# Performance work log

Hardware: AMD Instinct MI355X
Metric: run time of the kernel (lower is better)

The kernel has to match this reference:

```python
import jax, jax.numpy as jnp
import numpy as np

DIM = 256
DT_REF = 1.0
EPS = 1e-7
GATE_MIN, GATE_MAX = 0.01, 0.99


def _safe_forcing(exp_arg):
    # expm1(z)/z with denominator regularized by sign of real part (matches torch _safe_forcing)
    safe_denom = exp_arg + EPS * jnp.sign(exp_arg.real + EPS)
    return (jnp.exp(exp_arg) - 1.0) / safe_denom


def setup_inputs() -> dict:
    key = jax.random.key(0)
    ks = jax.random.split(key, 12)
    B, T, D = 8, 4096, DIM
    x_mean_seq = jax.random.normal(ks[0], (B, T, D), dtype=jnp.float32)
    dt_seq = jax.random.uniform(ks[1], (B, T), dtype=jnp.float32)
    # GlobalFluxTracker params
    decay_re = jax.random.normal(ks[2], (D,), dtype=jnp.float32) * 0.1 - 1.0
    decay_im = jax.random.normal(ks[3], (D,), dtype=jnp.float32) * 0.1
    W_in = jax.random.normal(ks[4], (2 * D, 2 * D), dtype=jnp.float32) * (1.0 / np.sqrt(2 * D))
    b_in = jnp.zeros((2 * D,), dtype=jnp.float32)
    W_out = jax.random.normal(ks[5], (2 * D, 2 * D), dtype=jnp.float32) * (1.0 / np.sqrt(2 * D))
    b_out = jnp.zeros((2 * D,), dtype=jnp.float32)
    W_gate = jax.random.normal(ks[6], (D, 2 * D), dtype=jnp.float32) * (1.0 / np.sqrt(2 * D))
    b_gate = jnp.zeros((D,), dtype=jnp.float32)
    # TemporalPropagator diagonal generator params
    lam_re = jax.random.normal(ks[7], (D,), dtype=jnp.float32) * 0.01
    lam_im = jax.random.normal(ks[8], (D,), dtype=jnp.float32) * 0.1
    return {
        "x_mean_seq": x_mean_seq, "dt_seq": dt_seq,
        "decay_re": decay_re, "decay_im": decay_im,
        "W_in": W_in, "b_in": b_in, "W_out": W_out, "b_out": b_out,
        "W_gate": W_gate, "b_gate": b_gate,
        "lam_re": lam_re, "lam_im": lam_im,
    }


def reference(x_mean_seq, dt_seq, decay_re, decay_im, W_in, b_in,
              W_out, b_out, W_gate, b_gate, lam_re, lam_im):
    # dt ratio [B,T,1]
    dt_ratio = (dt_seq / DT_REF)[..., None]

    # --- GlobalFluxTracker.get_scan_operators ---
    lam_f = -jax.nn.softplus(decay_re) + 1j * decay_im          # [D] complex64
    exp_arg = lam_f[None, None, :] * dt_ratio                    # [B,T,D]
    decay = jnp.exp(exp_arg)                                     # [B,T,D]
    forcing = _safe_forcing(exp_arg)                             # [B,T,D]

    # _mix_input on real input (imag part is zero)
    x_cat = jnp.concatenate([x_mean_seq, jnp.zeros_like(x_mean_seq)], axis=-1)
    x_in = x_cat @ W_in.T + b_in                                 # [B,T,2D]
    x_re, x_im = jnp.split(x_in, 2, axis=-1)
    x_mixed = x_re + 1j * x_im                                   # [B,T,D]
    X_scan = x_mixed * forcing                                   # [B,T,D]

    # --- linear recurrence flux_t = decay_t * flux_{t-1} + X_t (associative scan over T) ---
    def combine(c1, c2):
        a1, b1 = c1
        a2, b2 = c2
        return (a1 * a2, b1 * a2 + b2)
    _, flux = jax.lax.associative_scan(combine, (decay, X_scan), axis=1)  # [B,T,D]

    # --- compute_output_seq ---
    s_cat = jnp.concatenate([flux.real, flux.imag], axis=-1)     # [B,T,2D]
    src = s_cat @ W_out.T + b_out
    src_re, src_im = jnp.split(src, 2, axis=-1)
    gate = jax.nn.sigmoid(s_cat @ W_gate.T + b_gate)
    gate = gate * (GATE_MAX - GATE_MIN) + GATE_MIN               # [B,T,D]

    # --- TemporalPropagator.get_transition_operators_seq ---
    lam_p = -jax.nn.softplus(lam_re) + 1j * lam_im
    exp_arg_p = lam_p[None, None, :] * dt_ratio
    decay_p = jnp.exp(exp_arg_p)
    forcing_p = _safe_forcing(exp_arg_p)

    out = jnp.concatenate([
        src_re, src_im, gate,
        decay_p.real, decay_p.imag, forcing_p.real, forcing_p.imag,
    ], axis=-1)                                                  # [B,T,7D]
    return out
```

## Files before the change

kernel.cpp:

```cpp
#include <hip/hip_runtime.h>
#include <math.h>

#define DD 256
#define TT 4096
#define NBATCH 8
#define BTOK 32768
#define EPSF 1e-7f

typedef __attribute__((ext_vector_type(4))) float f32x4;
typedef __attribute__((ext_vector_type(8))) short bf16x8;

__device__ __forceinline__ float softplusf(float x) {
  float e = __expf(-fabsf(x));
  return fmaxf(x, 0.f) + __logf(1.f + e);
}
__device__ __forceinline__ float bf2f(unsigned short u) {
  union { unsigned int i; float f; } v; v.i = ((unsigned int)u) << 16; return v.f;
}
__device__ __forceinline__ unsigned short f2bf(float f) {
  union { float f; unsigned int i; } v; v.f = f;
  unsigned int x = v.i;
  unsigned int lsb = (x >> 16) & 1u;
  x += 0x7fffu + lsb;
  return (unsigned short)(x >> 16);
}
__device__ __forceinline__ void decay_forcing(float are, float aim,
    float& dre, float& dim, float& fre, float& fim) {
  float e = __expf(are);
  float s = __sinf(aim), c = __cosf(aim);
  dre = e * c; dim = e * s;
  float sg = (are + EPSF >= 0.f) ? 1.f : -1.f;
  float denr = are + EPSF * sg;
  float deni = aim;
  float inv = __builtin_amdgcn_rcpf(denr * denr + deni * deni);
  float nr = dre - 1.f, ni = dim;
  fre = (nr * denr + ni * deni) * inv;
  fim = (ni * denr - nr * deni) * inv;
}
__device__ __forceinline__ void gl_lds16(const void* g, void* l) {
  __builtin_amdgcn_global_load_lds(
      (const __attribute__((address_space(1))) unsigned int*)g,
      (__attribute__((address_space(3))) unsigned int*)l, 16, 0, 0);
}

__global__ __launch_bounds__(256) void prep(
    const float* __restrict__ x, unsigned short* __restrict__ Xb,
    const float* __restrict__ Win, unsigned short* __restrict__ Wp1,
    const float* __restrict__ Wout, const float* __restrict__ Wgate,
    unsigned short* __restrict__ Wp3)
{
  const int bid = blockIdx.x;
  if (bid < 8192) {
    size_t i = ((size_t)bid * 256 + threadIdx.x) * 4;
    float4 v = *reinterpret_cast<const float4*>(&x[i]);
    ushort4 u;
    u.x = f2bf(v.x); u.y = f2bf(v.y); u.z = f2bf(v.z); u.w = f2bf(v.w);
    *reinterpret_cast<ushort4*>(&Xb[i]) = u;
  } else if (bid < 8704) {
    const int p = bid - 8192;
    const int k = threadIdx.x;
    const int g = p >> 5, r = p & 31;
    const int src = (r < 16) ? (g * 16 + r) : (256 + g * 16 + (r - 16));
    Wp1[(size_t)p * 256 + k] = f2bf(Win[(size_t)src * 512 + k]);
  } else {
    const int p = bid - 8704;
    const float* src = (p < 512) ? (Wout + (size_t)p * 512)
                                 : (Wgate + (size_t)(p - 512) * 512);
    Wp3[(size_t)p * 512 + threadIdx.x] = f2bf(src[threadIdx.x]);
    Wp3[(size_t)p * 512 + threadIdx.x + 256] = f2bf(src[threadIdx.x + 256]);
  }
}

__global__ __launch_bounds__(256) void k1_mfma(
    const unsigned short* __restrict__ Xb,
    const unsigned short* __restrict__ Wp,
    const float* __restrict__ bin, const float* __restrict__ dts,
    const float* __restrict__ decr, const float* __restrict__ deci,
    unsigned int* __restrict__ Xri)
{
  __shared__ __align__(16) unsigned short As[128 * 64];
  __shared__ __align__(16) unsigned short Bs[128 * 64];
  const int bx = blockIdx.x;
  const int wg = (bx & 7) * 128 + (bx >> 3);
  const int mt = wg >> 2, nt = wg & 3;
  const int m0 = mt * 128, n0 = nt * 128;
  const int tid = threadIdx.x;
  const int lane = tid & 63, wid = tid >> 6;
  const int wr = wid >> 1, wc = wid & 1;
  const int l15 = lane & 15, hi = lane >> 4;
  const int lrow = tid >> 3;
  const int sslot = (tid & 7) ^ (lrow & 7);
  f32x4 acc[4][4];
  f32x4 z = {0.f, 0.f, 0.f, 0.f};
#pragma unroll
  for (int i = 0; i < 4; ++i)
#pragma unroll
    for (int j = 0; j < 4; ++j) acc[i][j] = z;

  for (int k0 = 0; k0 < 256; k0 += 64) {
    __syncthreads();
#pragma unroll
    for (int c = 0; c < 4; ++c) {
      gl_lds16(&Xb[(size_t)(m0 + c * 32 + lrow) * 256 + k0 + sslot * 8],
               &As[c * 2048 + tid * 8]);
      gl_lds16(&Wp[(size_t)(n0 + c * 32 + lrow) * 256 + k0 + sslot * 8],
               &Bs[c * 2048 + tid * 8]);
    }
    __syncthreads();
#pragma unroll
    for (int kk = 0; kk < 2; ++kk) {
      bf16x8 af[4], bfr[4];
      const int rslot = ((kk * 4 + hi) ^ (l15 & 7)) * 8;
#pragma unroll
      for (int m = 0; m < 4; ++m)
        af[m] = *reinterpret_cast<const bf16x8*>(&As[(wr * 64 + m * 16 + l15) * 64 + rslot]);
#pragma unroll
      for (int n = 0; n < 4; ++n)
        bfr[n] = *reinterpret_cast<const bf16x8*>(&Bs[(wc * 64 + n * 16 + l15) * 64 + rslot]);
#pragma unroll
      for (int m = 0; m < 4; ++m)
#pragma unroll
        for (int n = 0; n < 4; ++n)
          acc[m][n] = __builtin_amdgcn_mfma_f32_16x16x32_bf16(af[m], bfr[n], acc[m][n], 0, 0, 0);
    }
  }

  const int pbase = n0 + wc * 64;
#pragma unroll
  for (int pr = 0; pr < 2; ++pr) {
    const int d = (pbase >> 1) + pr * 16 + l15;
    const float nre = -softplusf(decr[d]);
    const float di = deci[d];
    const float br = bin[d], bi = bin[d + 256];
#pragma unroll
    for (int m = 0; m < 4; ++m) {
#pragma unroll
      for (int r = 0; r < 4; ++r) {
        const int row = m0 + wr * 64 + m * 16 + hi * 4 + r;
        float xr = acc[m][2 * pr][r] + br;
        float xi = acc[m][2 * pr + 1][r] + bi;
        float dt = dts[row];
        float are = nre * dt, aim = di * dt;
        float dr_, dm_, fr_, fm_;
        decay_forcing(are, aim, dr_, dm_, fr_, fm_);
        unsigned int pk = (unsigned int)f2bf(xr * fr_ - xi * fm_)
                        | ((unsigned int)f2bf(xr * fm_ + xi * fr_) << 16);
        Xri[(size_t)row * DD + d] = pk;
      }
    }
  }
}

__global__ __launch_bounds__(256) void k2a_chunk(
    const unsigned int* __restrict__ Xri,
    const float* __restrict__ dts, const float* __restrict__ decr,
    const float* __restrict__ deci,
    float4* __restrict__ ops)
{
  const int bx = blockIdx.x;
  const int b = bx >> 6, c = bx & 63;
  const int d = threadIdx.x;
  __shared__ float sdt[64];
  if (threadIdx.x < 64) sdt[threadIdx.x] = dts[b * TT + c * 64 + threadIdx.x];
  const float nre = -softplusf(decr[d]);
  const float di = deci[d];
  __syncthreads();
  float Ar = 1.f, Ai = 0.f, Br = 0.f, Bi = 0.f;
  size_t base = (size_t)(b * TT + c * 64) * DD + d;
  for (int i = 0; i < 64; ++i) {
    float dt = sdt[i];
    float e = __expf(nre * dt);
    float s = __sinf(di * dt), cs = __cosf(di * dt);
    float ar = e * cs, ai = e * s;
    unsigned int pk = Xri[base]; base += DD;
    float xr = bf2f((unsigned short)(pk & 0xffffu));
    float xi = bf2f((unsigned short)(pk >> 16));
    float nAr = Ar * ar - Ai * ai, nAi = Ar * ai + Ai * ar;
    Ar = nAr; Ai = nAi;
    float nBr = Br * ar - Bi * ai + xr, nBi = Br * ai + Bi * ar + xi;
    Br = nBr; Bi = nBi;
  }
  ops[(size_t)bx * DD + d] = make_float4(Ar, Ai, Br, Bi);
}

__global__ __launch_bounds__(256) void k2c_apply(
    const unsigned int* __restrict__ Xri,
    const float* __restrict__ dts, const float* __restrict__ decr,
    const float* __restrict__ deci,
    const float4* __restrict__ ops,
    unsigned short* __restrict__ F)
{
  const int bx = blockIdx.x;
  const int b = bx >> 6, c = bx & 63;
  const int d = threadIdx.x;
  __shared__ float sdt[64];
  if (threadIdx.x < 64) sdt[threadIdx.x] = dts[b * TT + c * 64 + threadIdx.x];
  const float nre = -softplusf(decr[d]);
  const float di = deci[d];
  __syncthreads();

  float hr = 0.f, hi2 = 0.f;
  const size_t obase = (size_t)(b * 64) * DD + d;
  for (int c0 = 0; c0 < c; c0 += 8) {
    float4 oo[8];
#pragma unroll
    for (int j = 0; j < 8; ++j)
      oo[j] = (c0 + j < c) ? ops[obase + (size_t)(c0 + j) * DD]
                           : make_float4(1.f, 0.f, 0.f, 0.f);
#pragma unroll
    for (int j = 0; j < 8; ++j) {
      float nr = oo[j].x * hr - oo[j].y * hi2 + oo[j].z;
      float ni = oo[j].x * hi2 + oo[j].y * hr + oo[j].w;
      hr = nr; hi2 = ni;
    }
  }

  const int tok0 = b * TT + c * 64;
  size_t base = (size_t)tok0 * DD + d;
  for (int i = 0; i < 64; ++i) {
    float dt = sdt[i];
    float e = __expf(nre * dt);
    float s = __sinf(di * dt), cs = __cosf(di * dt);
    float ar = e * cs, ai = e * s;
    unsigned int pk = Xri[base]; base += DD;
    float xr = bf2f((unsigned short)(pk & 0xffffu));
    float xi = bf2f((unsigned short)(pk >> 16));
    float nr = ar * hr - ai * hi2 + xr;
    float ni = ar * hi2 + ai * hr + xi;
    hr = nr; hi2 = ni;
    size_t fb = (size_t)(tok0 + i) * 512 + d;
    F[fb] = f2bf(hr);
    F[fb + 256] = f2bf(hi2);
  }
}

__global__ __launch_bounds__(256) void k3k4(
    const unsigned short* __restrict__ F,
    const unsigned short* __restrict__ Wp,
    const float* __restrict__ bout, const float* __restrict__ bgate,
    const float* __restrict__ dts, const float* __restrict__ lre,
    const float* __restrict__ lim,
    float* __restrict__ out)
{
  __shared__ __align__(16) unsigned short As[128 * 64];
  __shared__ __align__(16) unsigned short Bs[128 * 64];

  const int q = blockIdx.x / 5, r5 = blockIdx.x % 5;

  if (r5 >= 3) {
    const int pb = q * 2 + (r5 - 3);
    const int d = threadIdx.x;
    const float nl = -softplusf(lre[d]);
    const float li = lim[d];
    const int tok0 = pb * 32;
#pragma unroll 4
    for (int i = 0; i < 32; ++i) {
      const int tok = tok0 + i;
      float dt = dts[tok];
      float dr, dm, fr, fm;
      decay_forcing(nl * dt, li * dt, dr, dm, fr, fm);
      float* o = out + (size_t)tok * 1792 + 768;
      o[d] = dr; o[256 + d] = dm; o[512 + d] = fr; o[768 + d] = fm;
    }
    return;
  }

  const int gw = q * 3 + r5;
  const int wg = (gw & 7) * 192 + (gw >> 3);
  const int mt = wg / 6, nt = wg % 6;
  const int m0 = mt * 128, n0 = nt * 128;
  const int tid = threadIdx.x;
  const int lane = tid & 63, wid = tid >> 6;
  const int wr = wid >> 1, wc = wid & 1;
  const int l15 = lane & 15, hi = lane >> 4;
  const int lrow = tid >> 3;
  const int sslot = (tid & 7) ^ (lrow & 7);
  f32x4 acc[4][4];
  f32x4 z = {0.f, 0.f, 0.f, 0.f};
#pragma unroll
  for (int i = 0; i < 4; ++i)
#pragma unroll
    for (int j = 0; j < 4; ++j) acc[i][j] = z;

  for (int k0 = 0; k0 < 512; k0 += 64) {
    __syncthreads();
#pragma unroll
    for (int c = 0; c < 4; ++c) {
      gl_lds16(&F[(size_t)(m0 + c * 32 + lrow) * 512 + k0 + sslot * 8],
               &As[c * 2048 + tid * 8]);
      gl_lds16(&Wp[(size_t)(n0 + c * 32 + lrow) * 512 + k0 + sslot * 8],
               &Bs[c * 2048 + tid * 8]);
    }
    __syncthreads();
#pragma unroll
    for (int kk = 0; kk < 2; ++kk) {
      bf16x8 af[4], bfr[4];
      const int rslot = ((kk * 4 + hi) ^ (l15 & 7)) * 8;
#pragma unroll
      for (int m = 0; m < 4; ++m)
        af[m] = *reinterpret_cast<const bf16x8*>(&As[(wr * 64 + m * 16 + l15) * 64 + rslot]);
#pragma unroll
      for (int n = 0; n < 4; ++n)
        bfr[n] = *reinterpret_cast<const bf16x8*>(&Bs[(wc * 64 + n * 16 + l15) * 64 + rslot]);
#pragma unroll
      for (int m = 0; m < 4; ++m)
#pragma unroll
        for (int n = 0; n < 4; ++n)
          acc[m][n] = __builtin_amdgcn_mfma_f32_16x16x32_bf16(af[m], bfr[n], acc[m][n], 0, 0, 0);
    }
  }

  const int nb = n0 + wc * 64;
  if (nb < 512) {
#pragma unroll
    for (int j = 0; j < 4; ++j) {
      const int col = nb + j * 16 + l15;
      const float bb = bout[col];
#pragma unroll
      for (int m = 0; m < 4; ++m)
#pragma unroll
        for (int r = 0; r < 4; ++r) {
          const int row = m0 + wr * 64 + m * 16 + hi * 4 + r;
          out[(size_t)row * 1792 + col] = acc[m][j][r] + bb;
        }
    }
  } else {
#pragma unroll
    for (int j = 0; j < 4; ++j) {
      const int col = nb + j * 16 + l15;
      const float bb = bgate[col - 512];
#pragma unroll
      for (int m = 0; m < 4; ++m)
#pragma unroll
        for (int r = 0; r < 4; ++r) {
          const int row = m0 + wr * 64 + m * 16 + hi * 4 + r;
          float g = __builtin_amdgcn_rcpf(1.f + __expf(-(acc[m][j][r] + bb)));
          out[(size_t)row * 1792 + col] = g * 0.98f + 0.01f;
        }
    }
  }
}

extern "C" void kernel_launch(void* const* d_in, const int* in_sizes, int n_in,
                              void* d_out, int out_size, void* d_ws, size_t ws_size,
                              hipStream_t stream)
{
  const float* x     = (const float*)d_in[0];
  const float* dts   = (const float*)d_in[1];
  const float* decr  = (const float*)d_in[2];
  const float* deci  = (const float*)d_in[3];
  const float* Win   = (const float*)d_in[4];
  const float* bin   = (const float*)d_in[5];
  const float* Wout  = (const float*)d_in[6];
  const float* bout  = (const float*)d_in[7];
  const float* Wgate = (const float*)d_in[8];
  const float* bgate = (const float*)d_in[9];
  const float* lre   = (const float*)d_in[10];
  const float* lim   = (const float*)d_in[11];
  float* out = (float*)d_out;
  char* ws = (char*)d_ws;

  unsigned short* F   = (unsigned short*)(ws);
  unsigned short* Xb  = (unsigned short*)(ws + (size_t)16 * 1024 * 1024);
  unsigned int*  Xri  = (unsigned int*)(ws + (size_t)32 * 1024 * 1024);
  unsigned short* Wp1 = (unsigned short*)(ws + (size_t)64 * 1024 * 1024);
  unsigned short* Wp3 = (unsigned short*)(ws + (size_t)64 * 1024 * 1024 + 262144);
  float4* ops = (float4*)(ws + (size_t)65 * 1024 * 1024);

  prep<<<9472, 256, 0, stream>>>(x, Xb, Win, Wp1, Wout, Wgate, Wp3);
  k1_mfma<<<1024, 256, 0, stream>>>(Xb, Wp1, bin, dts, decr, deci, Xri);
  k2a_chunk<<<512, 256, 0, stream>>>(Xri, dts, decr, deci, ops);
  k2c_apply<<<512, 256, 0, stream>>>(Xri, dts, decr, deci, ops, F);
  k3k4<<<2560, 256, 0, stream>>>(F, Wp3, bout, bgate, dts, lre, lim, out);
}
```

Baseline: 129.6 us.

## Fuse chunk scan and apply kernels using inter-block flag synchronization

Merges the two scan kernels into one. Each block computes its chunk's aggregate operator, publishes it with a release flag, then spins on the flags of earlier chunks before applying the carry-in and writing the flux. The 64 Xri values per thread are held in registers so the second pass does not reload them from global memory. This removes one kernel launch and a full re-read of Xri. In exchange it adds spin-wait latency and heavy register pressure, and it depends on all 512 blocks being co-resident to avoid deadlock.

New measurement: 152.4 us. +17.6%, slower.

```diff
diff --git a/kernel.cpp b/kernel.cpp
--- a/kernel.cpp
+++ b/kernel.cpp
@@ -151,11 +151,12 @@
   }
 }
 
-__global__ __launch_bounds__(256) void k2a_chunk(
+__global__ __launch_bounds__(256) void k2_scan(
     const unsigned int* __restrict__ Xri,
     const float* __restrict__ dts, const float* __restrict__ decr,
     const float* __restrict__ deci,
-    float4* __restrict__ ops)
+    float4* __restrict__ ops, unsigned int* __restrict__ flags,
+    unsigned short* __restrict__ F)
 {
   const int bx = blockIdx.x;
   const int b = bx >> 6, c = bx & 63;
@@ -165,38 +166,37 @@
   const float nre = -softplusf(decr[d]);
   const float di = deci[d];
   __syncthreads();
+
+  unsigned int xs[64];
+  const size_t gbase = (size_t)(b * TT + c * 64) * DD + d;
+#pragma unroll
+  for (int i = 0; i < 64; ++i) xs[i] = Xri[gbase + (size_t)i * DD];
+
   float Ar = 1.f, Ai = 0.f, Br = 0.f, Bi = 0.f;
-  size_t base = (size_t)(b * TT + c * 64) * DD + d;
+#pragma unroll
   for (int i = 0; i < 64; ++i) {
     float dt = sdt[i];
     float e = __expf(nre * dt);
     float s = __sinf(di * dt), cs = __cosf(di * dt);
     float ar = e * cs, ai = e * s;
-    unsigned int pk = Xri[base]; base += DD;
-    float xr = bf2f((unsigned short)(pk & 0xffffu));
-    float xi = bf2f((unsigned short)(pk >> 16));
+    float xr = bf2f((unsigned short)(xs[i] & 0xffffu));
+    float xi = bf2f((unsigned short)(xs[i] >> 16));
     float nAr = Ar * ar - Ai * ai, nAi = Ar * ai + Ai * ar;
     Ar = nAr; Ai = nAi;
     float nBr = Br * ar - Bi * ai + xr, nBi = Br * ai + Bi * ar + xi;
     Br = nBr; Bi = nBi;
   }
   ops[(size_t)bx * DD + d] = make_float4(Ar, Ai, Br, Bi);
-}
-
-__global__ __launch_bounds__(256) void k2c_apply(
-    const unsigned int* __restrict__ Xri,
-    const float* __restrict__ dts, const float* __restrict__ decr,
-    const float* __restrict__ deci,
-    const float4* __restrict__ ops,
-    unsigned short* __restrict__ F)
-{
-  const int bx = blockIdx.x;
-  const int b = bx >> 6, c = bx & 63;
-  const int d = threadIdx.x;
-  __shared__ float sdt[64];
-  if (threadIdx.x < 64) sdt[threadIdx.x] = dts[b * TT + c * 64 + threadIdx.x];
-  const float nre = -softplusf(decr[d]);
-  const float di = deci[d];
+  __syncthreads();
+  if (threadIdx.x == 0)
+    __hip_atomic_store(&flags[bx], 1u, __ATOMIC_RELEASE, __HIP_MEMORY_SCOPE_AGENT);
+
+  if (threadIdx.x < c) {
+    while (__hip_atomic_load(&flags[(b << 6) + threadIdx.x], __ATOMIC_ACQUIRE,
+                             __HIP_MEMORY_SCOPE_AGENT) == 0u) {
+      __builtin_amdgcn_s_sleep(2);
+    }
+  }
   __syncthreads();
 
   float hr = 0.f, hi2 = 0.f;
@@ -216,15 +216,14 @@
   }
 
   const int tok0 = b * TT + c * 64;
-  size_t base = (size_t)tok0 * DD + d;
+#pragma unroll
   for (int i = 0; i < 64; ++i) {
     float dt = sdt[i];
     float e = __expf(nre * dt);
     float s = __sinf(di * dt), cs = __cosf(di * dt);
     float ar = e * cs, ai = e * s;
-    unsigned int pk = Xri[base]; base += DD;
-    float xr = bf2f((unsigned short)(pk & 0xffffu));
-    float xi = bf2f((unsigned short)(pk >> 16));
+    float xr = bf2f((unsigned short)(xs[i] & 0xffffu));
+    float xi = bf2f((unsigned short)(xs[i] >> 16));
     float nr = ar * hr - ai * hi2 + xr;
     float ni = ar * hi2 + ai * hr + xi;
     hr = nr; hi2 = ni;
@@ -366,10 +365,11 @@
   unsigned short* Wp1 = (unsigned short*)(ws + (size_t)64 * 1024 * 1024);
   unsigned short* Wp3 = (unsigned short*)(ws + (size_t)64 * 1024 * 1024 + 262144);
   float4* ops = (float4*)(ws + (size_t)65 * 1024 * 1024);
-
+  unsigned int* flags = (unsigned int*)(ws + (size_t)67 * 1024 * 1024);
+
+  hipMemsetAsync(flags, 0, 512 * sizeof(unsigned int), stream);
   prep<<<9472, 256, 0, stream>>>(x, Xb, Win, Wp1, Wout, Wgate, Wp3);
   k1_mfma<<<1024, 256, 0, stream>>>(Xb, Wp1, bin, dts, decr, deci, Xri);
-  k2a_chunk<<<512, 256, 0, stream>>>(Xri, dts, decr, deci, ops);
-  k2c_apply<<<512, 256, 0, stream>>>(Xri, dts, decr, deci, ops, F);
+  k2_scan<<<512, 256, 0, stream>>>(Xri, dts, decr, deci, ops, flags, F);
   k3k4<<<2560, 256, 0, stream>>>(F, Wp3, bout, bgate, dts, lre, lim, out);
 }
```
